# Kernel tuning notes

Hardware: AMD Instinct MI355X
Metric: run time of the kernel (lower is better)

## Reference

```python
import jax, jax.numpy as jnp
import numpy as np

USAGE_DECAY = 0.99
EPS = 1e-12


def _addressing(key, beta, gate, shift, gamma, prev_w, memory, half_shift):
    # key [B,M], beta/gate/gamma [B,1], shift [B,K], prev_w [B,N], memory [B,N,M]
    kn = key / (jnp.linalg.norm(key, axis=-1, keepdims=True) + EPS)
    mn = memory / (jnp.linalg.norm(memory, axis=-1, keepdims=True) + EPS)
    cos = jnp.einsum('bnm,bm->bn', mn, kn)                      # [B,N]
    beta_p = jax.nn.softplus(beta[:, 0])
    wc = jax.nn.softmax(beta_p[:, None] * cos, axis=-1)
    g = jax.nn.sigmoid(gate[:, 0])[:, None]
    wg = g * wc + (1.0 - g) * prev_w
    s = jax.nn.softmax(shift, axis=-1)                          # [B,K]
    K = shift.shape[-1]
    shifted = sum(s[:, k:k + 1] * jnp.roll(wg, k - half_shift, axis=-1) for k in range(K))
    gamma_p = 1.0 + jax.nn.softplus(gamma[:, 0])
    wt = (shifted + EPS) ** gamma_p[:, None]
    return wt / (wt.sum(axis=-1, keepdims=True) + EPS)


def _allocate(usage):
    # faithful to source: cumprod over zero-prepended shifted usage
    sorted_u = jnp.sort(usage, axis=-1)
    free = jnp.argsort(usage, axis=-1)
    shifted = jnp.concatenate([jnp.zeros_like(sorted_u[:, :1]), sorted_u[:, :-1]], axis=-1)
    aw = (1.0 - sorted_u) * jnp.cumprod(shifted, axis=-1)
    B = usage.shape[0]
    return jnp.zeros_like(usage).at[jnp.arange(B)[:, None], free].set(aw)


def _forward(ctrl, read_W, read_b, write_W, write_b,
             memory0, link0, precedence0, usage0, read_w0, write_w0):
    T, B, D = ctrl.shape
    N, M = memory0.shape[1], memory0.shape[2]
    RH, WH = read_w0.shape[1], write_w0.shape[1]
    rpl = read_W.shape[0] // RH   # M + K + 6
    wpl = write_W.shape[0] // WH  # 3M + K + 4
    K = rpl - M - 6
    half = K // 2
    eye = jnp.eye(N, dtype=memory0.dtype)

    def step(carry, ctrl_t):
        memory, link, prec, usage, read_w, write_w = carry
        rp = (ctrl_t @ read_W.T + read_b).reshape(B, RH, rpl)
        wp = (ctrl_t @ write_W.T + write_b).reshape(B, WH, wpl)

        # ---- write heads: content addr + allocation, erase/add, temporal links ----
        new_write = []
        for h in range(WH):
            p = wp[:, h]
            key = p[:, :M]
            beta = p[:, M:M + 1]
            gate = p[:, M + 1:M + 2]
            shift = p[:, M + 2:M + 2 + K]
            gamma = p[:, M + 2 + K:M + 3 + K]
            erase = jax.nn.sigmoid(p[:, M + 3 + K:2 * M + 3 + K])
            add = p[:, 2 * M + 3 + K:3 * M + 3 + K]
            a_gate = jax.nn.sigmoid(p[:, 3 * M + 3 + K:])          # [B,1]
            w_addr = _addressing(key, beta, gate, shift, gamma, write_w[:, h], memory, half)
            alloc = _allocate(usage)
            w = a_gate * alloc + (1.0 - a_gate) * w_addr           # [B,N]
            memory = memory * (1.0 - w[:, :, None] * erase[:, None, :]) + w[:, :, None] * add[:, None, :]
            link = (1.0 - w[:, :, None]) * link + prec[:, :, None] * w[:, None, :]
            link = link * (1.0 - eye)[None]
            # faithful to source: sum over dim 0 (batch)
            prec = (1.0 - w.sum(axis=0, keepdims=True)) * prec + w
            usage = jnp.clip(USAGE_DECAY * usage + w, 0.0, 1.0)
            new_write.append(w)
        write_w = jnp.stack(new_write, axis=1)

        # ---- read heads: content + forward/backward temporal link modes ----
        new_read, reads = [], []
        for h in range(RH):
            p = rp[:, h]
            key = p[:, :M]
            beta = p[:, M:M + 1]
            gate = p[:, M + 1:M + 2]
            shift = p[:, M + 2:M + 2 + K]
            gamma = p[:, M + 2 + K:M + 3 + K]
            pi = jax.nn.softmax(p[:, M + 3 + K:M + 6 + K], axis=-1)  # [B,3] back/content/fwd
            wc = _addressing(key, beta, gate, shift, gamma, read_w[:, h], memory, half)
            fwd = jnp.einsum('bn,bnk->bk', read_w[:, h], link)
            bwd = jnp.einsum('bn,bkn->bk', read_w[:, h], link)
            w = pi[:, 0:1] * bwd + pi[:, 1:2] * wc + pi[:, 2:3] * fwd
            new_read.append(w)
            reads.append(jnp.einsum('bn,bnm->bm', w, memory))
        read_w = jnp.stack(new_read, axis=1)
        reads = jnp.stack(reads, axis=1)                            # [B,RH,M]
        return (memory, link, prec, usage, read_w, write_w), reads

    carry0 = (memory0, link0, precedence0, usage0, read_w0, write_w0)
    _, reads = jax.lax.scan(step, carry0, ctrl)
    return reads  # [T,B,RH,M]


def setup_inputs() -> dict:
    key = jax.random.key(0)
    ks = jax.random.split(key, 8)
    T, B, D = 32, 4, 256
    N, M = 1024, 256
    RH, WH, K = 1, 1, 3
    rpl = M + K + 6
    wpl = 3 * M + K + 4
    ctrl = jax.random.normal(ks[0], (T, B, D), dtype=jnp.float32)
    read_W = jax.random.normal(ks[1], (RH * rpl, D), dtype=jnp.float32) * 0.05
    read_b = jnp.zeros((RH * rpl,), dtype=jnp.float32)
    write_W = jax.random.normal(ks[2], (WH * wpl, D), dtype=jnp.float32) * 0.05
    write_b = jnp.zeros((WH * wpl,), dtype=jnp.float32)
    memory0 = jax.random.normal(ks[3], (B, N, M), dtype=jnp.float32) * 0.1
    link0 = jnp.zeros((B, N, N), dtype=jnp.float32)
    precedence0 = jnp.zeros((B, N), dtype=jnp.float32)
    usage0 = jax.random.uniform(ks[4], (B, N), dtype=jnp.float32)
    read_w0 = jnp.zeros((B, RH, N), dtype=jnp.float32).at[:, :, 0].set(1.0)
    write_w0 = jnp.zeros((B, WH, N), dtype=jnp.float32).at[:, :, 0].set(1.0)
    return {"ctrl": ctrl, "read_W": read_W, "read_b": read_b,
            "write_W": write_W, "write_b": write_b, "memory0": memory0,
            "link0": link0, "precedence0": precedence0, "usage0": usage0,
            "read_w0": read_w0, "write_w0": write_w0}


def reference(ctrl, read_W, read_b, write_W, write_b, memory0, link0,
              precedence0, usage0, read_w0, write_w0):
    return _forward(ctrl, read_W, read_b, write_W, write_b,
                    memory0, link0, precedence0, usage0, read_w0, write_w0)
```

## Files before the change

### kernel.cpp

```cpp
#include <hip/hip_runtime.h>

#define GRID 128
#define TPB 256
#define SLICE 32
#define BB 4
#define DD 256
#define NN 1024
#define MM 256
#define KSH 3
#define RPL 265
#define WPL 775
#define TS 32
#define EPSF 1e-12f

struct KArgs {
    const float *ctrl, *rW, *rb, *wW, *wb;
    const float *memory0, *prec0, *read_w0, *write_w0;
    float *out;
    float *rp, *wp;
    float *cosr, *cosw, *wbuf, *rdw;
    float *csp, *dsp;
    float *rdp;
    unsigned *flagsA, *flagsB;
};

__device__ __forceinline__ float cload(const float* p){
    return __hip_atomic_load(p, __ATOMIC_RELAXED, __HIP_MEMORY_SCOPE_SYSTEM);
}
__device__ __forceinline__ void cstore(float* p, float v){
    __hip_atomic_store(p, v, __ATOMIC_RELAXED, __HIP_MEMORY_SCOPE_SYSTEM);
}

__device__ __forceinline__ float softplusf(float x){
    return fmaxf(x, 0.0f) + log1pf(expf(-fabsf(x)));
}
__device__ __forceinline__ float sigmoidf(float x){
    return 1.0f / (1.0f + expf(-x));
}

template <bool FENCE>
__device__ __forceinline__ void garrive(unsigned* flags, unsigned gen, int g, int tid){
    __syncthreads();
    if (tid == 0){
        if (FENCE) __builtin_amdgcn_fence(__ATOMIC_RELEASE, "agent");
        __hip_atomic_store(&flags[g*16], gen, __ATOMIC_RELAXED, __HIP_MEMORY_SCOPE_SYSTEM);
    }
}
template <bool FENCE>
__device__ __forceinline__ void gwait(unsigned* flags, unsigned gen, int tid){
    if (tid < 64){
        while (1){
            unsigned f0 = __hip_atomic_load(&flags[tid*16], __ATOMIC_RELAXED, __HIP_MEMORY_SCOPE_SYSTEM);
            unsigned f1 = __hip_atomic_load(&flags[(tid+64)*16], __ATOMIC_RELAXED, __HIP_MEMORY_SCOPE_SYSTEM);
            if (__all(f0 >= gen && f1 >= gen)) break;
            __builtin_amdgcn_s_sleep(1);
        }
    }
    __syncthreads();
    if (FENCE) __builtin_amdgcn_fence(__ATOMIC_ACQUIRE, "agent");
    asm volatile("" ::: "memory");
}

__device__ __forceinline__ float blk_sum(float v, float* s4, int tid){
    #pragma unroll
    for (int off = 32; off; off >>= 1) v += __shfl_down(v, off);
    if ((tid & 63) == 0) s4[tid >> 6] = v;
    __syncthreads();
    float r = s4[0] + s4[1] + s4[2] + s4[3];
    __syncthreads();
    return r;
}
__device__ __forceinline__ float blk_max(float v, float* s4, int tid){
    #pragma unroll
    for (int off = 32; off; off >>= 1) v = fmaxf(v, __shfl_down(v, off));
    if ((tid & 63) == 0) s4[tid >> 6] = v;
    __syncthreads();
    float r = fmaxf(fmaxf(s4[0], s4[1]), fmaxf(s4[2], s4[3]));
    __syncthreads();
    return r;
}
__device__ __forceinline__ float half_sum(float v, float* slots, int htid){
    #pragma unroll
    for (int off = 32; off; off >>= 1) v += __shfl_down(v, off);
    if ((htid & 63) == 0) slots[htid >> 6] = v;
    __syncthreads();
    float r = slots[0] + slots[1];
    __syncthreads();
    return r;
}

__device__ __forceinline__ void addr_core2(const float cosx[4], const float prev[4],
                                           const float* __restrict__ p,
                                           float* s4, float* wg, int tid,
                                           float out_wc[4]){
    float beta_p  = softplusf(p[MM]);
    float g       = sigmoidf(p[MM+1]);
    float s0r = p[MM+2], s1r = p[MM+3], s2r = p[MM+4];
    float smx = fmaxf(s0r, fmaxf(s1r, s2r));
    float e0 = expf(s0r-smx), e1 = expf(s1r-smx), e2 = expf(s2r-smx);
    float sden = e0+e1+e2;
    float s0 = e0/sden, s1 = e1/sden, s2 = e2/sden;
    float gamma_p = 1.0f + softplusf(p[MM+2+KSH]);
    float ev[4]; float ls = 0.0f;
    #pragma unroll
    for (int q = 0; q < 4; q++){ ev[q] = expf(beta_p*cosx[q] - beta_p); ls += ev[q]; }
    float bs = blk_sum(ls, s4, tid);
    float invb = 1.0f / bs;
    #pragma unroll
    for (int q = 0; q < 4; q++){
        int i = tid + q*256;
        wg[i] = g*(ev[q]*invb) + (1.0f-g)*prev[q];
    }
    __syncthreads();
    float wt[4]; float lps = 0.0f;
    #pragma unroll
    for (int q = 0; q < 4; q++){
        int i = tid + q*256;
        float sh = s0*wg[(i+1)&(NN-1)] + s1*wg[i] + s2*wg[(i-1)&(NN-1)];
        wt[q] = exp2f(gamma_p * log2f(sh + EPSF));
        lps += wt[q];
    }
    float ts = blk_sum(lps, s4, tid);
    float inv = 1.0f / (ts + EPSF);
    #pragma unroll
    for (int q = 0; q < 4; q++) out_wc[q] = wt[q] * inv;
    __syncthreads();
}

__device__ __forceinline__ void addr_half(const float cosx[8], const float prev[8],
                                          const float* __restrict__ p,
                                          float* swg, float* slots,
                                          int htid, float out_wc[8]){
    float beta_p  = softplusf(p[MM]);
    float g       = sigmoidf(p[MM+1]);
    float s0r = p[MM+2], s1r = p[MM+3], s2r = p[MM+4];
    float smx = fmaxf(s0r, fmaxf(s1r, s2r));
    float e0 = expf(s0r-smx), e1 = expf(s1r-smx), e2 = expf(s2r-smx);
    float sden = e0+e1+e2;
    float s0 = e0/sden, s1 = e1/sden, s2 = e2/sden;
    float gamma_p = 1.0f + softplusf(p[MM+2+KSH]);

    float ev[8]; float ls = 0.0f;
    #pragma unroll
    for (int q = 0; q < 8; q++){ ev[q] = expf(beta_p*cosx[q] - beta_p); ls += ev[q]; }
    float bs = half_sum(ls, slots, htid);
    float invb = 1.0f / bs;
    #pragma unroll
    for (int q = 0; q < 8; q++){
        int i = htid + q*128;
        swg[i] = g*(ev[q]*invb) + (1.0f-g)*prev[q];
    }
    __syncthreads();
    float wt[8]; float lps = 0.0f;
    #pragma unroll
    for (int q = 0; q < 8; q++){
        int i = htid + q*128;
        float sh = s0*swg[(i+1)&(NN-1)] + s1*swg[i] + s2*swg[(i-1)&(NN-1)];
        wt[q] = exp2f(gamma_p * log2f(sh + EPSF));
        lps += wt[q];
    }
    float ts2 = half_sum(lps, slots, htid);
    float inv = 1.0f / (ts2 + EPSF);
    #pragma unroll
    for (int q = 0; q < 8; q++) out_wc[q] = wt[q] * inv;
    __syncthreads();
}

__device__ __forceinline__ void tail_cos(const KArgs& a, int tnext, int b, int g, int ns0,
        float (*lmem)[MM], float (*skey)[MM],
        const float* lwn, const float* rdvec, int tid){
    if (rdvec){
        float accv = 0.f;
        #pragma unroll 8
        for (int j = 0; j < SLICE; j++) accv += rdvec[j]*lmem[j][tid];
        cstore(&a.rdp[(size_t)((tnext-1)&1)*GRID*MM + g*MM + tid], accv);
    }
    const float* kr = a.rp + (size_t)tnext*BB*RPL + (size_t)b*RPL;
    const bool hw = (tnext+1 <= TS-1);
    const float* kwp = a.wp + (size_t)(hw ? tnext+1 : tnext)*BB*WPL + (size_t)b*WPL;
    skey[0][tid] = kr[tid];
    skey[1][tid] = kwp[tid];
    __syncthreads();
    {
        const float* pw = a.wp + (size_t)tnext*BB*WPL + (size_t)b*WPL;
        float e = pw[MM+3+KSH + tid];
        float d = pw[2*MM+3+KSH + tid];
        #pragma unroll 8
        for (int j = 0; j < SLICE; j++){
            float w = lwn[j];
            lmem[j][tid] = lmem[j][tid]*(1.0f - w*e) + w*d;
        }
    }
    __syncthreads();
    {
        int j = tid >> 3, c = tid & 7;
        float dr=0.f, dw=0.f, nm=0.f, nr=0.f, nk=0.f;
        #pragma unroll
        for (int m = 0; m < 8; m++){
            int col = c*4 + m*32;
            float4 mv = *(const float4*)&lmem[j][col];
            float4 rv = *(const float4*)&skey[0][col];
            float4 wv = *(const float4*)&skey[1][col];
            dr += mv.x*rv.x + mv.y*rv.y + mv.z*rv.z + mv.w*rv.w;
            dw += mv.x*wv.x + mv.y*wv.y + mv.z*wv.z + mv.w*wv.w;
            nm += mv.x*mv.x + mv.y*mv.y + mv.z*mv.z + mv.w*mv.w;
            nr += rv.x*rv.x + rv.y*rv.y + rv.z*rv.z + rv.w*rv.w;
            nk += wv.x*wv.x + wv.y*wv.y + wv.z*wv.z + wv.w*wv.w;
        }
        #pragma unroll
        for (int off = 4; off; off >>= 1){
            dr += __shfl_down(dr, off); dw += __shfl_down(dw, off);
            nm += __shfl_down(nm, off); nr += __shfl_down(nr, off);
            nk += __shfl_down(nk, off);
        }
        if (c == 0){
            float sn = sqrtf(nm) + EPSF;
            int n = ns0 + j;
            cstore(&a.cosr[(size_t)(tnext&1)*BB*NN + b*NN + n], dr/(sn*(sqrtf(nr)+EPSF)));
            if (hw) cstore(&a.cosw[(size_t)((tnext+1)&1)*BB*NN + b*NN + n], dw/(sn*(sqrtf(nk)+EPSF)));
        }
    }
}

__device__ __forceinline__ void tail_links(const KArgs& a, int tnext, int g,
        float (*lA)[SLICE], float (*lW)[SLICE],
        const float* lwn, const float* rvec, const float* lprec, int tid){
    for (int p2 = tid; p2 < tnext*SLICE; p2 += TPB){
        int s = p2 >> 5, jj = p2 & 31;
        lA[s][jj] *= (1.0f - lwn[jj]);
    }
    __syncthreads();
    if (tid < SLICE){ lA[tnext][tid] = lprec[tid]; lW[tnext][tid] = lwn[tid]; }
    __syncthreads();
    int s = tid >> 3, c = tid & 7;
    if (s <= tnext){
        float pc = 0.f, pd = 0.f;
        #pragma unroll
        for (int q = 0; q < 4; q++){
            int jj = c*4 + q;
            float r = rvec[jj];
            pc += r*lA[s][jj];
            pd += r*lW[s][jj];
        }
        #pragma unroll
        for (int off = 4; off; off >>= 1){ pc += __shfl_down(pc, off); pd += __shfl_down(pd, off); }
        if (c == 0){
            cstore(&a.csp[(size_t)(tnext&1)*GRID*TS + g*TS + s], pc);
            cstore(&a.dsp[(size_t)(tnext&1)*GRID*TS + g*TS + s], pd);
        }
    }
}

__global__ void __launch_bounds__(TPB) kfull(KArgs a){
    const int g   = blockIdx.x;
    const int tid = threadIdx.x;
    const int wvi = tid >> 6, lane = tid & 63;
    const int b   = g >> 5;
    const int sl  = g & 31;
    const int ns0 = sl * SLICE;
    const int sq    = sl >> 3;
    const int sbase = (sl & 7) * 32;
    const int hbase = ns0 & 127;
    const int qsl   = ns0 >> 7;

    __shared__ __align__(16) float lmem[SLICE][MM];
    __shared__ __align__(16) float skey[2][MM];
    __shared__ __align__(16) float lA[TS][SLICE];
    __shared__ __align__(16) float lW[TS][SLICE];
    __shared__ float wgA[NN], wgB[NN];
    __shared__ float s8[8];
    __shared__ float scs[TS], sds[TS];
    __shared__ float lprec[SLICE], lr_old[SLICE], lw_old[SLICE];
    __shared__ float lrn[SLICE], lwn[SLICE], lbw[SLICE], lfw[SLICE];

    {
        const int tt = g >> 2;
        for (int o = tid; o < BB*DD; o += TPB) wgA[o] = a.ctrl[(size_t)tt*BB*DD + o];
        __syncthreads();
        for (int half = 0; half < 2; half++){
            int jc = (g & 3) + half*4;
            int j = jc*130 + tid;
            if (tid < 130 && j < RPL + WPL){
                const float* wrow; float bias; int isw, jj;
                if (j < RPL){ jj = j;       wrow = a.rW + (size_t)jj*DD; bias = a.rb[jj]; isw = 0; }
                else        { jj = j - RPL; wrow = a.wW + (size_t)jj*DD; bias = a.wb[jj]; isw = 1; }
                const float4* w4 = (const float4*)wrow;
                float a0 = bias, a1 = bias, a2 = bias, a3 = bias;
                for (int d = 0; d < DD/4; d++){
                    float4 wv = w4[d];
                    float4 c0 = *(const float4*)&wgA[0*DD + d*4];
                    float4 c1 = *(const float4*)&wgA[1*DD + d*4];
                    float4 c2 = *(const float4*)&wgA[2*DD + d*4];
                    float4 c3 = *(const float4*)&wgA[3*DD + d*4];
                    a0 += wv.x*c0.x + wv.y*c0.y + wv.z*c0.z + wv.w*c0.w;
                    a1 += wv.x*c1.x + wv.y*c1.y + wv.z*c1.z + wv.w*c1.w;
                    a2 += wv.x*c2.x + wv.y*c2.y + wv.z*c2.z + wv.w*c2.w;
                    a3 += wv.x*c3.x + wv.y*c3.y + wv.z*c3.z + wv.w*c3.w;
                }
                if (isw && jj >= MM+3+KSH && jj < 2*MM+3+KSH){
                    a0 = sigmoidf(a0); a1 = sigmoidf(a1); a2 = sigmoidf(a2); a3 = sigmoidf(a3);
                }
                if (!isw){
                    float* dst = a.rp + (size_t)tt*BB*RPL;
                    dst[0*RPL+jj]=a0; dst[1*RPL+jj]=a1; dst[2*RPL+jj]=a2; dst[3*RPL+jj]=a3;
                } else {
                    float* dst = a.wp + (size_t)tt*BB*WPL;
                    dst[0*WPL+jj]=a0; dst[1*WPL+jj]=a1; dst[2*WPL+jj]=a2; dst[3*WPL+jj]=a3;
                }
            }
        }
    }
    garrive<true>(a.flagsA, 1, g, tid);
    gwait<true>(a.flagsA, 1, tid);

    {
        const float* kw = a.wp + (size_t)b*WPL;
        const int m0 = lane*4;
        float k0=kw[m0], k1=kw[m0+1], k2=kw[m0+2], k3=kw[m0+3];
        float nk = k0*k0 + k1*k1 + k2*k2 + k3*k3;
        #pragma unroll
        for (int off = 32; off; off >>= 1) nk += __shfl_down(nk, off);
        nk = __shfl(nk, 0);
        float snk = sqrtf(nk) + EPSF;
        for (int rr = 0; rr < 8; rr++){
            int j = wvi*8 + rr, n = ns0 + j;
            float4 m4 = ((const float4*)a.memory0)[((size_t)(b*NN+n))*64 + lane];
            *(float4*)&lmem[j][m0] = m4;
            float dw = m4.x*k0 + m4.y*k1 + m4.z*k2 + m4.w*k3;
            float nm = m4.x*m4.x + m4.y*m4.y + m4.z*m4.z + m4.w*m4.w;
            #pragma unroll
            for (int off = 32; off; off >>= 1){ dw += __shfl_down(dw, off); nm += __shfl_down(nm, off); }
            if (lane == 0) cstore(&a.cosw[0*BB*NN + b*NN + n], dw / ((sqrtf(nm)+EPSF)*snk));
        }
        if (tid < SLICE){
            lprec[tid]  = a.prec0[b*NN + ns0 + tid];
            lr_old[tid] = a.read_w0[b*NN + ns0 + tid];
        }
    }
    garrive<false>(a.flagsA, 2, g, tid);
    gwait<false>(a.flagsA, 2, tid);

    {
        const float* p = a.wp + (size_t)b*WPL;
        float cosx[4], prev[4], wcf[4];
        #pragma unroll
        for (int q = 0; q < 4; q++){
            int i = tid + q*256;
            cosx[q] = cload(&a.cosw[0*BB*NN + b*NN + i]);
            prev[q] = a.write_w0[b*NN + i];
        }
        addr_core2(cosx, prev, p, s8, wgA, tid, wcf);
        float ag = sigmoidf(p[3*MM+3+KSH]);
        if (tid >= sbase && tid < sbase+32){
            int j = tid - sbase;
            float v = (1.0f - ag)*wcf[sq];
            lwn[j] = v;
            cstore(&a.wbuf[0*BB*NN + b*NN + ns0 + j], v);
        }
        __syncthreads();
        tail_cos(a, 0, b, g, ns0, lmem, skey, lwn, nullptr, tid);
        garrive<false>(a.flagsA, 3, g, tid);
        tail_links(a, 0, g, lA, lW, lwn, lr_old, lprec, tid);
        garrive<false>(a.flagsB, 1, g, tid);
        __syncthreads();
        if (tid < SLICE) lw_old[tid] = lwn[tid];
    }

    for (int t = 0; t < TS; t++){
        const int cur = t & 1, nxt = cur ^ 1;
        const int half = wvi >> 1, htid = tid & 127;
        gwait<false>(a.flagsA, 3 + t, tid);

        float cosx[8], prev[8];
        const float* addr_p;
        if (half == 0){
            addr_p = a.rp + (size_t)t*BB*RPL + (size_t)b*RPL;
            #pragma unroll
            for (int q = 0; q < 8; q++){
                int i = htid + q*128;
                cosx[q] = cload(&a.cosr[(size_t)cur*BB*NN + b*NN + i]);
                prev[q] = (t == 0) ? a.read_w0[b*NN + i]
                                   : cload(&a.rdw[(size_t)nxt*BB*NN + b*NN + i]);
            }
        } else {
            int tw = (t < TS-1) ? t+1 : t;
            addr_p = a.wp + (size_t)tw*BB*WPL + (size_t)b*WPL;
            #pragma unroll
            for (int q = 0; q < 8; q++){
                int i = htid + q*128;
                cosx[q] = cload(&a.cosw[(size_t)nxt*BB*NN + b*NN + i]);
                prev[q] = cload(&a.wbuf[(size_t)cur*BB*NN + b*NN + i]);
            }
        }
        if (tid < SLICE){
            float wsum = 0.f;
            #pragma unroll
            for (int bq = 0; bq < BB; bq++)
                wsum += cload(&a.wbuf[(size_t)cur*BB*NN + bq*NN + ns0 + tid]);
            lprec[tid] = (1.0f - wsum)*lprec[tid] + lw_old[tid];
        }

        float wcf[8];
        addr_half(cosx, prev, addr_p,
                  (half == 0) ? wgA : wgB,
                  (half == 0) ? &s8[0] : &s8[2],
                  htid, wcf);

        gwait<false>(a.flagsB, 1 + t, tid);

        {
            int s = tid >> 3, c = tid & 7;
            float pc = 0.f, pd = 0.f;
            if (s <= t){
                #pragma unroll
                for (int q = 0; q < 4; q++){
                    int slc = c + q*8;
                    pc += cload(&a.csp[(size_t)cur*GRID*TS + (b*32+slc)*TS + s]);
                    pd += cload(&a.dsp[(size_t)cur*GRID*TS + (b*32+slc)*TS + s]);
                }
            }
            float rdpv = 0.f;
            if (t > 0)
                rdpv = cload(&a.rdp[(size_t)nxt*GRID*MM + (b*32+(tid&31))*MM + sl*8 + (tid>>5)]);
            #pragma unroll
            for (int off = 4; off; off >>= 1){ pc += __shfl_down(pc, off); pd += __shfl_down(pd, off); }
            if (c == 0 && s <= t){ scs[s] = pc; sds[s] = pd; }
            if (t > 0){
                #pragma unroll
                for (int off = 16; off; off >>= 1) rdpv += __shfl_down(rdpv, off);
                if ((tid & 31) == 0) a.out[(size_t)(t-1)*BB*MM + b*MM + sl*8 + (tid>>5)] = rdpv;
            }
        }
        __syncthreads();
        if (tid < SLICE){
            float bwv = 0.f, fwv = 0.f, qq = 0.f;
            for (int s2 = 0; s2 <= t; s2++){
                float av = lA[s2][tid], wv = lW[s2][tid];
                qq  += av*wv;
                bwv += sds[s2]*av;
                fwv += scs[s2]*wv;
            }
            float corr = lr_old[tid]*qq;
            lbw[tid] = bwv - corr;
            lfw[tid] = fwv - corr;
        }
        __syncthreads();
        if (half == 0){
            float x0 = addr_p[MM+3+KSH], x1 = addr_p[MM+4+KSH], x2 = addr_p[MM+5+KSH];
            float mx = fmaxf(x0, fmaxf(x1, x2));
            float q0 = expf(x0-mx), q1 = expf(x1-mx), q2 = expf(x2-mx);
            float qs = q0+q1+q2;
            float pi0 = q0/qs, pi1 = q1/qs, pi2 = q2/qs;
            if (htid >= hbase && htid < hbase + 32){
                int j = htid - hbase;
                float v = pi0*lbw[j] + pi1*wcf[qsl] + pi2*lfw[j];
                lrn[j] = v;
                cstore(&a.rdw[(size_t)cur*BB*NN + b*NN + ns0 + j], v);
            }
        } else if (t < TS-1){
            float ag = sigmoidf(addr_p[3*MM+3+KSH]);
            if (htid >= hbase && htid < hbase + 32){
                int j = htid - hbase;
                float v = (1.0f - ag)*wcf[qsl];
                lwn[j] = v;
                cstore(&a.wbuf[(size_t)nxt*BB*NN + b*NN + ns0 + j], v);
            }
        }
        __syncthreads();

        if (t < TS-1){
            tail_cos(a, t+1, b, g, ns0, lmem, skey, lwn, lrn, tid);
            garrive<false>(a.flagsA, 4 + t, g, tid);
            tail_links(a, t+1, g, lA, lW, lwn, lrn, lprec, tid);
            garrive<false>(a.flagsB, 2 + t, g, tid);
            __syncthreads();
            if (tid < SLICE){ lr_old[tid] = lrn[tid]; lw_old[tid] = lwn[tid]; }
        } else {
            float accv = 0.f;
            #pragma unroll 8
            for (int j = 0; j < SLICE; j++) accv += lrn[j]*lmem[j][tid];
            cstore(&a.rdp[(size_t)1*GRID*MM + g*MM + tid], accv);
            garrive<false>(a.flagsB, 2 + t, g, tid);
        }
    }

    gwait<false>(a.flagsB, TS + 1, tid);
    {
        float v = cload(&a.rdp[(size_t)1*GRID*MM + (b*32+(tid&31))*MM + sl*8 + (tid>>5)]);
        #pragma unroll
        for (int off = 16; off; off >>= 1) v += __shfl_down(v, off);
        if ((tid & 31) == 0) a.out[(size_t)(TS-1)*BB*MM + b*MM + sl*8 + (tid>>5)] = v;
    }
}

extern "C" void kernel_launch(void* const* d_in, const int* in_sizes, int n_in,
                              void* d_out, int out_size, void* d_ws, size_t ws_size,
                              hipStream_t stream) {
    KArgs ka;
    ka.ctrl     = (const float*)d_in[0];
    ka.rW       = (const float*)d_in[1];
    ka.rb       = (const float*)d_in[2];
    ka.wW       = (const float*)d_in[3];
    ka.wb       = (const float*)d_in[4];
    ka.memory0  = (const float*)d_in[5];
    ka.prec0    = (const float*)d_in[7];
    ka.read_w0  = (const float*)d_in[9];
    ka.write_w0 = (const float*)d_in[10];
    ka.out      = (float*)d_out;

    float* ws = (float*)d_ws;
    size_t off = 0;
    auto alloc = [&](size_t n){ float* p = ws + off; off += n; return p; };
    ka.rp    = alloc((size_t)TS*BB*RPL);
    ka.wp    = alloc((size_t)TS*BB*WPL);
    ka.cosr  = alloc(2*(size_t)BB*NN);
    ka.cosw  = alloc(2*(size_t)BB*NN);
    ka.wbuf  = alloc(2*(size_t)BB*NN);
    ka.rdw   = alloc(2*(size_t)BB*NN);
    ka.csp   = alloc(2*(size_t)GRID*TS);
    ka.dsp   = alloc(2*(size_t)GRID*TS);
    ka.rdp   = alloc(2*(size_t)GRID*MM);
    unsigned* ubase = (unsigned*)(ws + off);
    ka.flagsA = ubase;
    ka.flagsB = ubase + GRID*16;
    size_t bar_bytes = (2*GRID*16) * sizeof(unsigned);

    hipMemsetAsync((void*)ubase, 0, bar_bytes, stream);
    void* params[] = { &ka };
    hipLaunchCooperativeKernel((const void*)kfull, dim3(GRID), dim3(TPB), params, 0, stream);
}
```

Measured before the change: 332.7 us.

## Cut block barriers and restructure per-step tail loops in persistent DNC kernel

Removes several __syncthreads by giving the addressing reductions separate shared slots and merging the link decay/insert passes into one loop. The read-vector partial product is fused into the memory erase/add update, which now uses float4 rows split across waves; this writes four partial rdp rows per block, and consumers sum them. The cosine computation is remapped to 32-lane reductions over rows, and the link readout is spread across all threads with a shuffle reduction instead of 32 threads looping. Link arrays are padded to 33 columns to avoid LDS bank conflicts. The cost is more global partial stores and loads, and relying on barriers being correctly placed after their removal.

```diff
diff --git a/kernel.cpp b/kernel.cpp
--- a/kernel.cpp
+++ b/kernel.cpp
@@ -12,6 +12,7 @@
 #define WPL 775
 #define TS 32
 #define EPSF 1e-12f
+#define SLP 33
 
 struct KArgs {
     const float *ctrl, *rW, *rb, *wW, *wb;
@@ -70,23 +71,13 @@
     __syncthreads();
     return r;
 }
-__device__ __forceinline__ float blk_max(float v, float* s4, int tid){
-    #pragma unroll
-    for (int off = 32; off; off >>= 1) v = fmaxf(v, __shfl_down(v, off));
-    if ((tid & 63) == 0) s4[tid >> 6] = v;
-    __syncthreads();
-    float r = fmaxf(fmaxf(s4[0], s4[1]), fmaxf(s4[2], s4[3]));
-    __syncthreads();
-    return r;
-}
-__device__ __forceinline__ float half_sum(float v, float* slots, int htid){
+
+__device__ __forceinline__ float half_sum1(float v, float* slot2, int htid){
     #pragma unroll
     for (int off = 32; off; off >>= 1) v += __shfl_down(v, off);
-    if ((htid & 63) == 0) slots[htid >> 6] = v;
-    __syncthreads();
-    float r = slots[0] + slots[1];
-    __syncthreads();
-    return r;
+    if ((htid & 63) == 0) slot2[htid >> 6] = v;
+    __syncthreads();
+    return slot2[0] + slot2[1];
 }
 
 __device__ __forceinline__ void addr_core2(const float cosx[4], const float prev[4],
@@ -129,7 +120,7 @@
 
 __device__ __forceinline__ void addr_half(const float cosx[8], const float prev[8],
                                           const float* __restrict__ p,
-                                          float* swg, float* slots,
+                                          float* swg, float* slot_bs, float* slot_ts,
                                           int htid, float out_wc[8]){
     float beta_p  = softplusf(p[MM]);
     float g       = sigmoidf(p[MM+1]);
@@ -143,7 +134,7 @@
     float ev[8]; float ls = 0.0f;
     #pragma unroll
     for (int q = 0; q < 8; q++){ ev[q] = expf(beta_p*cosx[q] - beta_p); ls += ev[q]; }
-    float bs = half_sum(ls, slots, htid);
+    float bs = half_sum1(ls, slot_bs, htid);
     float invb = 1.0f / bs;
     #pragma unroll
     for (int q = 0; q < 8; q++){
@@ -159,23 +150,17 @@
         wt[q] = exp2f(gamma_p * log2f(sh + EPSF));
         lps += wt[q];
     }
-    float ts2 = half_sum(lps, slots, htid);
+    float ts2 = half_sum1(lps, slot_ts, htid);
     float inv = 1.0f / (ts2 + EPSF);
     #pragma unroll
     for (int q = 0; q < 8; q++) out_wc[q] = wt[q] * inv;
-    __syncthreads();
-}
-
-__device__ __forceinline__ void tail_cos(const KArgs& a, int tnext, int b, int g, int ns0,
+}
+
+__device__ __forceinline__ void tail_cos2(const KArgs& a, int tnext, int b, int g, int ns0,
         float (*lmem)[MM], float (*skey)[MM],
-        const float* lwn, const float* rdvec, int tid){
-    if (rdvec){
-        float accv = 0.f;
-        #pragma unroll 8
-        for (int j = 0; j < SLICE; j++) accv += rdvec[j]*lmem[j][tid];
-        cstore(&a.rdp[(size_t)((tnext-1)&1)*GRID*MM + g*MM + tid], accv);
-    }
-    const float* kr = a.rp + (size_t)tnext*BB*RPL + (size_t)b*RPL;
+        const float* lwn, const float* rdvec,
+        int tid, int wvi){
+    const float* kr  = a.rp + (size_t)tnext*BB*RPL + (size_t)b*RPL;
     const bool hw = (tnext+1 <= TS-1);
     const float* kwp = a.wp + (size_t)(hw ? tnext+1 : tnext)*BB*WPL + (size_t)b*WPL;
     skey[0][tid] = kr[tid];
@@ -183,54 +168,81 @@
     __syncthreads();
     {
         const float* pw = a.wp + (size_t)tnext*BB*WPL + (size_t)b*WPL;
-        float e = pw[MM+3+KSH + tid];
-        float d = pw[2*MM+3+KSH + tid];
-        #pragma unroll 8
-        for (int j = 0; j < SLICE; j++){
+        const int quad = tid & 63;
+        float eX[4], dX[4];
+        #pragma unroll
+        for (int k = 0; k < 4; k++){
+            eX[k] = pw[MM+3+KSH   + quad*4 + k];
+            dX[k] = pw[2*MM+3+KSH + quad*4 + k];
+        }
+        float4 acc = make_float4(0.f,0.f,0.f,0.f);
+        #pragma unroll
+        for (int it = 0; it < 8; it++){
+            int j = wvi + it*4;
             float w = lwn[j];
-            lmem[j][tid] = lmem[j][tid]*(1.0f - w*e) + w*d;
+            float4 mv = *(float4*)&lmem[j][quad*4];
+            if (rdvec){
+                float r = rdvec[j];
+                acc.x += r*mv.x; acc.y += r*mv.y; acc.z += r*mv.z; acc.w += r*mv.w;
+            }
+            mv.x = mv.x*(1.0f - w*eX[0]) + w*dX[0];
+            mv.y = mv.y*(1.0f - w*eX[1]) + w*dX[1];
+            mv.z = mv.z*(1.0f - w*eX[2]) + w*dX[2];
+            mv.w = mv.w*(1.0f - w*eX[3]) + w*dX[3];
+            *(float4*)&lmem[j][quad*4] = mv;
+        }
+        if (rdvec){
+            float* base = a.rdp + (size_t)((tnext-1)&1)*GRID*4*MM + (size_t)g*4*MM + wvi*MM + quad*4;
+            cstore(base+0, acc.x); cstore(base+1, acc.y);
+            cstore(base+2, acc.z); cstore(base+3, acc.w);
         }
     }
     __syncthreads();
     {
-        int j = tid >> 3, c = tid & 7;
-        float dr=0.f, dw=0.f, nm=0.f, nr=0.f, nk=0.f;
+        const int cc = tid & 31, jb = tid >> 5;
+        float nr = 0.f, nk = 0.f;
         #pragma unroll
         for (int m = 0; m < 8; m++){
-            int col = c*4 + m*32;
-            float4 mv = *(const float4*)&lmem[j][col];
-            float4 rv = *(const float4*)&skey[0][col];
-            float4 wv = *(const float4*)&skey[1][col];
-            dr += mv.x*rv.x + mv.y*rv.y + mv.z*rv.z + mv.w*rv.w;
-            dw += mv.x*wv.x + mv.y*wv.y + mv.z*wv.z + mv.w*wv.w;
-            nm += mv.x*mv.x + mv.y*mv.y + mv.z*mv.z + mv.w*mv.w;
-            nr += rv.x*rv.x + rv.y*rv.y + rv.z*rv.z + rv.w*rv.w;
-            nk += wv.x*wv.x + wv.y*wv.y + wv.z*wv.z + wv.w*wv.w;
-        }
-        #pragma unroll
-        for (int off = 4; off; off >>= 1){
-            dr += __shfl_down(dr, off); dw += __shfl_down(dw, off);
-            nm += __shfl_down(nm, off); nr += __shfl_down(nr, off);
-            nk += __shfl_down(nk, off);
-        }
-        if (c == 0){
-            float sn = sqrtf(nm) + EPSF;
-            int n = ns0 + j;
-            cstore(&a.cosr[(size_t)(tnext&1)*BB*NN + b*NN + n], dr/(sn*(sqrtf(nr)+EPSF)));
-            if (hw) cstore(&a.cosw[(size_t)((tnext+1)&1)*BB*NN + b*NN + n], dw/(sn*(sqrtf(nk)+EPSF)));
-        }
-    }
-}
-
-__device__ __forceinline__ void tail_links(const KArgs& a, int tnext, int g,
-        float (*lA)[SLICE], float (*lW)[SLICE],
+            int col = cc + m*32;
+            float rv = skey[0][col], wv = skey[1][col];
+            nr += rv*rv; nk += wv*wv;
+        }
+        #pragma unroll
+        for (int off = 16; off; off >>= 1){ nr += __shfl_down(nr, off); nk += __shfl_down(nk, off); }
+        #pragma unroll
+        for (int rb = 0; rb < 4; rb++){
+            int j = jb + rb*8;
+            float dr = 0.f, dw = 0.f, nm = 0.f;
+            #pragma unroll
+            for (int m = 0; m < 8; m++){
+                int col = cc + m*32;
+                float mv = lmem[j][col];
+                dr += mv*skey[0][col];
+                dw += mv*skey[1][col];
+                nm += mv*mv;
+            }
+            #pragma unroll
+            for (int off = 16; off; off >>= 1){
+                dr += __shfl_down(dr, off); dw += __shfl_down(dw, off); nm += __shfl_down(nm, off);
+            }
+            if (cc == 0){
+                float sn = sqrtf(nm) + EPSF;
+                int n = ns0 + j;
+                cstore(&a.cosr[(size_t)(tnext&1)*BB*NN + b*NN + n], dr/(sn*(sqrtf(nr)+EPSF)));
+                if (hw) cstore(&a.cosw[(size_t)((tnext+1)&1)*BB*NN + b*NN + n], dw/(sn*(sqrtf(nk)+EPSF)));
+            }
+        }
+    }
+}
+
+__device__ __forceinline__ void tail_links2(const KArgs& a, int tnext, int g,
+        float (*lA)[SLP], float (*lW)[SLP],
         const float* lwn, const float* rvec, const float* lprec, int tid){
-    for (int p2 = tid; p2 < tnext*SLICE; p2 += TPB){
+    for (int p2 = tid; p2 < (tnext+1)*SLICE; p2 += TPB){
         int s = p2 >> 5, jj = p2 & 31;
-        lA[s][jj] *= (1.0f - lwn[jj]);
-    }
-    __syncthreads();
-    if (tid < SLICE){ lA[tnext][tid] = lprec[tid]; lW[tnext][tid] = lwn[tid]; }
+        if (s == tnext){ lA[s][jj] = lprec[jj]; lW[s][jj] = lwn[jj]; }
+        else            lA[s][jj] *= (1.0f - lwn[jj]);
+    }
     __syncthreads();
     int s = tid >> 3, c = tid & 7;
     if (s <= tnext){
@@ -265,8 +277,8 @@
 
     __shared__ __align__(16) float lmem[SLICE][MM];
     __shared__ __align__(16) float skey[2][MM];
-    __shared__ __align__(16) float lA[TS][SLICE];
-    __shared__ __align__(16) float lW[TS][SLICE];
+    __shared__ float lA[TS][SLP];
+    __shared__ float lW[TS][SLP];
     __shared__ float wgA[NN], wgB[NN];
     __shared__ float s8[8];
     __shared__ float scs[TS], sds[TS];
@@ -357,13 +369,11 @@
             lwn[j] = v;
             cstore(&a.wbuf[0*BB*NN + b*NN + ns0 + j], v);
         }
-        __syncthreads();
-        tail_cos(a, 0, b, g, ns0, lmem, skey, lwn, nullptr, tid);
+        tail_cos2(a, 0, b, g, ns0, lmem, skey, lwn, nullptr, tid, wvi);
+        if (tid < SLICE) lw_old[tid] = lwn[tid];
         garrive<false>(a.flagsA, 3, g, tid);
-        tail_links(a, 0, g, lA, lW, lwn, lr_old, lprec, tid);
+        tail_links2(a, 0, g, lA, lW, lwn, lr_old, lprec, tid);
         garrive<false>(a.flagsB, 1, g, tid);
-        __syncthreads();
-        if (tid < SLICE) lw_old[tid] = lwn[tid];
     }
 
     for (int t = 0; t < TS; t++){
@@ -404,6 +414,7 @@
         addr_half(cosx, prev, addr_p,
                   (half == 0) ? wgA : wgB,
                   (half == 0) ? &s8[0] : &s8[2],
+                  (half == 0) ? &s8[4] : &s8[6],
                   htid, wcf);
 
         gwait<false>(a.flagsB, 1 + t, tid);
@@ -420,8 +431,12 @@
                 }
             }
             float rdpv = 0.f;
-            if (t > 0)
-                rdpv = cload(&a.rdp[(size_t)nxt*GRID*MM + (b*32+(tid&31))*MM + sl*8 + (tid>>5)]);
+            if (t > 0){
+                int slc = tid & 31, ci = tid >> 5;
+                const float* base = a.rdp + (size_t)nxt*GRID*4*MM + (size_t)(b*32+slc)*4*MM + sl*8 + ci;
+                #pragma unroll
+                for (int f = 0; f < 4; f++) rdpv += cload(base + f*MM);
+            }
             #pragma unroll
             for (int off = 4; off; off >>= 1){ pc += __shfl_down(pc, off); pd += __shfl_down(pd, off); }
             if (c == 0 && s <= t){ scs[s] = pc; sds[s] = pd; }
@@ -432,17 +447,22 @@
             }
         }
         __syncthreads();
-        if (tid < SLICE){
+        {
+            int j2 = tid >> 3, c2 = tid & 7;
             float bwv = 0.f, fwv = 0.f, qq = 0.f;
-            for (int s2 = 0; s2 <= t; s2++){
-                float av = lA[s2][tid], wv = lW[s2][tid];
-                qq  += av*wv;
-                bwv += sds[s2]*av;
-                fwv += scs[s2]*wv;
-            }
-            float corr = lr_old[tid]*qq;
-            lbw[tid] = bwv - corr;
-            lfw[tid] = fwv - corr;
+            for (int s2 = c2; s2 <= t; s2 += 8){
+                float av = lA[s2][j2], wv = lW[s2][j2];
+                qq += av*wv; bwv += sds[s2]*av; fwv += scs[s2]*wv;
+            }
+            #pragma unroll
+            for (int off = 4; off; off >>= 1){
+                bwv += __shfl_down(bwv, off); fwv += __shfl_down(fwv, off); qq += __shfl_down(qq, off);
+            }
+            if (c2 == 0){
+                float corr = lr_old[j2]*qq;
+                lbw[j2] = bwv - corr;
+                lfw[j2] = fwv - corr;
+            }
         }
         __syncthreads();
         if (half == 0){
@@ -466,30 +486,41 @@
                 cstore(&a.wbuf[(size_t)nxt*BB*NN + b*NN + ns0 + j], v);
             }
         }
-        __syncthreads();
 
         if (t < TS-1){
-            tail_cos(a, t+1, b, g, ns0, lmem, skey, lwn, lrn, tid);
+            tail_cos2(a, t+1, b, g, ns0, lmem, skey, lwn, lrn, tid, wvi);
+            if (tid < SLICE){ lr_old[tid] = lrn[tid]; lw_old[tid] = lwn[tid]; }
             garrive<false>(a.flagsA, 4 + t, g, tid);
-            tail_links(a, t+1, g, lA, lW, lwn, lrn, lprec, tid);
+            tail_links2(a, t+1, g, lA, lW, lwn, lrn, lprec, tid);
             garrive<false>(a.flagsB, 2 + t, g, tid);
+        } else {
             __syncthreads();
-            if (tid < SLICE){ lr_old[tid] = lrn[tid]; lw_old[tid] = lwn[tid]; }
-        } else {
-            float accv = 0.f;
-            #pragma unroll 8
-            for (int j = 0; j < SLICE; j++) accv += lrn[j]*lmem[j][tid];
-            cstore(&a.rdp[(size_t)1*GRID*MM + g*MM + tid], accv);
+            const int quad = tid & 63;
+            float4 acc = make_float4(0.f,0.f,0.f,0.f);
+            #pragma unroll
+            for (int it = 0; it < 8; it++){
+                int j = wvi + it*4;
+                float r = lrn[j];
+                float4 mv = *(float4*)&lmem[j][quad*4];
+                acc.x += r*mv.x; acc.y += r*mv.y; acc.z += r*mv.z; acc.w += r*mv.w;
+            }
+            float* base = a.rdp + (size_t)1*GRID*4*MM + (size_t)g*4*MM + wvi*MM + quad*4;
+            cstore(base+0, acc.x); cstore(base+1, acc.y);
+            cstore(base+2, acc.z); cstore(base+3, acc.w);
             garrive<false>(a.flagsB, 2 + t, g, tid);
         }
     }
 
     gwait<false>(a.flagsB, TS + 1, tid);
     {
-        float v = cload(&a.rdp[(size_t)1*GRID*MM + (b*32+(tid&31))*MM + sl*8 + (tid>>5)]);
+        int slc = tid & 31, ci = tid >> 5;
+        const float* base = a.rdp + (size_t)1*GRID*4*MM + (size_t)(b*32+slc)*4*MM + sl*8 + ci;
+        float v = 0.f;
+        #pragma unroll
+        for (int f = 0; f < 4; f++) v += cload(base + f*MM);
         #pragma unroll
         for (int off = 16; off; off >>= 1) v += __shfl_down(v, off);
-        if ((tid & 31) == 0) a.out[(size_t)(TS-1)*BB*MM + b*MM + sl*8 + (tid>>5)] = v;
+        if ((tid & 31) == 0) a.out[(size_t)(TS-1)*BB*MM + b*MM + sl*8 + ci] = v;
     }
 }
 
@@ -519,7 +550,7 @@
     ka.rdw   = alloc(2*(size_t)BB*NN);
     ka.csp   = alloc(2*(size_t)GRID*TS);
     ka.dsp   = alloc(2*(size_t)GRID*TS);
-    ka.rdp   = alloc(2*(size_t)GRID*MM);
+    ka.rdp   = alloc(2*(size_t)GRID*4*MM);
     unsigned* ubase = (unsigned*)(ws + off);
     ka.flagsA = ubase;
     ka.flagsB = ubase + GRID*16;
```

Result: slower. 383.6 us (+15.3%).

## Halve grid to 64 blocks of 512 threads with 64-row memory slices

Applied to the files above, without the earlier changes.

Repartitions the persistent cooperative kernel from 128 blocks of 256 threads to 64 blocks of 512 threads, each owning a 64-row memory slice. Read and write addressing now run on two 256-thread teams in parallel. Grid barriers poll half as many flags, and the cross-block partial reductions shrink. The flagsB wait and the global loads of link and read partials are moved before addressing, and the read-vector accumulation is fused into the memory update loop. The cost is more shared memory per block and fewer CUs in use.

```diff
diff --git a/kernel.cpp b/kernel.cpp
--- a/kernel.cpp
+++ b/kernel.cpp
@@ -1,8 +1,8 @@
 #include <hip/hip_runtime.h>
 
-#define GRID 128
-#define TPB 256
-#define SLICE 32
+#define GRID 64
+#define TPB 512
+#define SLICE 64
 #define BB 4
 #define DD 256
 #define NN 1024
@@ -51,8 +51,7 @@
     if (tid < 64){
         while (1){
             unsigned f0 = __hip_atomic_load(&flags[tid*16], __ATOMIC_RELAXED, __HIP_MEMORY_SCOPE_SYSTEM);
-            unsigned f1 = __hip_atomic_load(&flags[(tid+64)*16], __ATOMIC_RELAXED, __HIP_MEMORY_SCOPE_SYSTEM);
-            if (__all(f0 >= gen && f1 >= gen)) break;
+            if (__all(f0 >= gen)) break;
             __builtin_amdgcn_s_sleep(1);
         }
     }
@@ -61,38 +60,18 @@
     asm volatile("" ::: "memory");
 }
 
-__device__ __forceinline__ float blk_sum(float v, float* s4, int tid){
+__device__ __forceinline__ float team_sum(float v, float* slot4, int ttid){
     #pragma unroll
     for (int off = 32; off; off >>= 1) v += __shfl_down(v, off);
-    if ((tid & 63) == 0) s4[tid >> 6] = v;
-    __syncthreads();
-    float r = s4[0] + s4[1] + s4[2] + s4[3];
-    __syncthreads();
-    return r;
-}
-__device__ __forceinline__ float blk_max(float v, float* s4, int tid){
-    #pragma unroll
-    for (int off = 32; off; off >>= 1) v = fmaxf(v, __shfl_down(v, off));
-    if ((tid & 63) == 0) s4[tid >> 6] = v;
-    __syncthreads();
-    float r = fmaxf(fmaxf(s4[0], s4[1]), fmaxf(s4[2], s4[3]));
-    __syncthreads();
-    return r;
-}
-__device__ __forceinline__ float half_sum(float v, float* slots, int htid){
-    #pragma unroll
-    for (int off = 32; off; off >>= 1) v += __shfl_down(v, off);
-    if ((htid & 63) == 0) slots[htid >> 6] = v;
-    __syncthreads();
-    float r = slots[0] + slots[1];
-    __syncthreads();
-    return r;
-}
-
-__device__ __forceinline__ void addr_core2(const float cosx[4], const float prev[4],
-                                           const float* __restrict__ p,
-                                           float* s4, float* wg, int tid,
-                                           float out_wc[4]){
+    if ((ttid & 63) == 0) slot4[ttid >> 6] = v;
+    __syncthreads();
+    return slot4[0] + slot4[1] + slot4[2] + slot4[3];
+}
+
+__device__ __forceinline__ void addr_team(const float cosx[4], const float prev[4],
+                                          const float* __restrict__ p,
+                                          float* swg, float* slot_bs, float* slot_ts,
+                                          int ttid, float out_wc[4]){
     float beta_p  = softplusf(p[MM]);
     float g       = sigmoidf(p[MM+1]);
     float s0r = p[MM+2], s1r = p[MM+3], s2r = p[MM+4];
@@ -104,94 +83,56 @@
     float ev[4]; float ls = 0.0f;
     #pragma unroll
     for (int q = 0; q < 4; q++){ ev[q] = expf(beta_p*cosx[q] - beta_p); ls += ev[q]; }
-    float bs = blk_sum(ls, s4, tid);
+    float bs = team_sum(ls, slot_bs, ttid);
     float invb = 1.0f / bs;
     #pragma unroll
     for (int q = 0; q < 4; q++){
-        int i = tid + q*256;
-        wg[i] = g*(ev[q]*invb) + (1.0f-g)*prev[q];
+        int i = ttid + q*256;
+        swg[i] = g*(ev[q]*invb) + (1.0f-g)*prev[q];
     }
     __syncthreads();
     float wt[4]; float lps = 0.0f;
     #pragma unroll
     for (int q = 0; q < 4; q++){
-        int i = tid + q*256;
-        float sh = s0*wg[(i+1)&(NN-1)] + s1*wg[i] + s2*wg[(i-1)&(NN-1)];
-        wt[q] = exp2f(gamma_p * log2f(sh + EPSF));
-        lps += wt[q];
-    }
-    float ts = blk_sum(lps, s4, tid);
-    float inv = 1.0f / (ts + EPSF);
-    #pragma unroll
-    for (int q = 0; q < 4; q++) out_wc[q] = wt[q] * inv;
-    __syncthreads();
-}
-
-__device__ __forceinline__ void addr_half(const float cosx[8], const float prev[8],
-                                          const float* __restrict__ p,
-                                          float* swg, float* slots,
-                                          int htid, float out_wc[8]){
-    float beta_p  = softplusf(p[MM]);
-    float g       = sigmoidf(p[MM+1]);
-    float s0r = p[MM+2], s1r = p[MM+3], s2r = p[MM+4];
-    float smx = fmaxf(s0r, fmaxf(s1r, s2r));
-    float e0 = expf(s0r-smx), e1 = expf(s1r-smx), e2 = expf(s2r-smx);
-    float sden = e0+e1+e2;
-    float s0 = e0/sden, s1 = e1/sden, s2 = e2/sden;
-    float gamma_p = 1.0f + softplusf(p[MM+2+KSH]);
-
-    float ev[8]; float ls = 0.0f;
-    #pragma unroll
-    for (int q = 0; q < 8; q++){ ev[q] = expf(beta_p*cosx[q] - beta_p); ls += ev[q]; }
-    float bs = half_sum(ls, slots, htid);
-    float invb = 1.0f / bs;
-    #pragma unroll
-    for (int q = 0; q < 8; q++){
-        int i = htid + q*128;
-        swg[i] = g*(ev[q]*invb) + (1.0f-g)*prev[q];
-    }
-    __syncthreads();
-    float wt[8]; float lps = 0.0f;
-    #pragma unroll
-    for (int q = 0; q < 8; q++){
-        int i = htid + q*128;
+        int i = ttid + q*256;
         float sh = s0*swg[(i+1)&(NN-1)] + s1*swg[i] + s2*swg[(i-1)&(NN-1)];
         wt[q] = exp2f(gamma_p * log2f(sh + EPSF));
         lps += wt[q];
     }
-    float ts2 = half_sum(lps, slots, htid);
+    float ts2 = team_sum(lps, slot_ts, ttid);
     float inv = 1.0f / (ts2 + EPSF);
     #pragma unroll
-    for (int q = 0; q < 8; q++) out_wc[q] = wt[q] * inv;
-    __syncthreads();
+    for (int q = 0; q < 4; q++) out_wc[q] = wt[q] * inv;
 }
 
 __device__ __forceinline__ void tail_cos(const KArgs& a, int tnext, int b, int g, int ns0,
-        float (*lmem)[MM], float (*skey)[MM],
+        float (*lmem)[MM], float (*skey)[MM], float* wred,
         const float* lwn, const float* rdvec, int tid){
-    if (rdvec){
-        float accv = 0.f;
-        #pragma unroll 8
-        for (int j = 0; j < SLICE; j++) accv += rdvec[j]*lmem[j][tid];
-        cstore(&a.rdp[(size_t)((tnext-1)&1)*GRID*MM + g*MM + tid], accv);
-    }
     const float* kr = a.rp + (size_t)tnext*BB*RPL + (size_t)b*RPL;
     const bool hw = (tnext+1 <= TS-1);
     const float* kwp = a.wp + (size_t)(hw ? tnext+1 : tnext)*BB*WPL + (size_t)b*WPL;
-    skey[0][tid] = kr[tid];
-    skey[1][tid] = kwp[tid];
+    if (tid < 256) skey[0][tid] = kr[tid];
+    else           skey[1][tid-256] = kwp[tid-256];
     __syncthreads();
     {
+        const int col = tid & 255, rg = tid >> 8;
         const float* pw = a.wp + (size_t)tnext*BB*WPL + (size_t)b*WPL;
-        float e = pw[MM+3+KSH + tid];
-        float d = pw[2*MM+3+KSH + tid];
+        float e = pw[MM+3+KSH + col];
+        float d = pw[2*MM+3+KSH + col];
+        float accv = 0.f;
         #pragma unroll 8
-        for (int j = 0; j < SLICE; j++){
+        for (int k = 0; k < 32; k++){
+            int j = rg*32 + k;
             float w = lwn[j];
-            lmem[j][tid] = lmem[j][tid]*(1.0f - w*e) + w*d;
-        }
-    }
-    __syncthreads();
+            float mv = lmem[j][col];
+            if (rdvec) accv += rdvec[j]*mv;
+            lmem[j][col] = mv*(1.0f - w*e) + w*d;
+        }
+        if (rdvec) wred[rg*256 + col] = accv;
+    }
+    __syncthreads();
+    if (rdvec && tid < 256)
+        cstore(&a.rdp[(size_t)((tnext-1)&1)*GRID*MM + g*MM + tid], wred[tid] + wred[256+tid]);
     {
         int j = tid >> 3, c = tid & 7;
         float dr=0.f, dw=0.f, nm=0.f, nr=0.f, nk=0.f;
@@ -226,7 +167,7 @@
         float (*lA)[SLICE], float (*lW)[SLICE],
         const float* lwn, const float* rvec, const float* lprec, int tid){
     for (int p2 = tid; p2 < tnext*SLICE; p2 += TPB){
-        int s = p2 >> 5, jj = p2 & 31;
+        int s = p2 >> 6, jj = p2 & 63;
         lA[s][jj] *= (1.0f - lwn[jj]);
     }
     __syncthreads();
@@ -236,8 +177,8 @@
     if (s <= tnext){
         float pc = 0.f, pd = 0.f;
         #pragma unroll
-        for (int q = 0; q < 4; q++){
-            int jj = c*4 + q;
+        for (int q = 0; q < 8; q++){
+            int jj = c*8 + q;
             float r = rvec[jj];
             pc += r*lA[s][jj];
             pd += r*lW[s][jj];
@@ -255,32 +196,29 @@
     const int g   = blockIdx.x;
     const int tid = threadIdx.x;
     const int wvi = tid >> 6, lane = tid & 63;
-    const int b   = g >> 5;
-    const int sl  = g & 31;
+    const int b   = g >> 4;
+    const int sl  = g & 15;
     const int ns0 = sl * SLICE;
-    const int sq    = sl >> 3;
-    const int sbase = (sl & 7) * 32;
-    const int hbase = ns0 & 127;
-    const int qsl   = ns0 >> 7;
+    const int qsl   = ns0 >> 8;
+    const int hbase = ns0 & 255;
 
     __shared__ __align__(16) float lmem[SLICE][MM];
     __shared__ __align__(16) float skey[2][MM];
     __shared__ __align__(16) float lA[TS][SLICE];
     __shared__ __align__(16) float lW[TS][SLICE];
-    __shared__ float wgA[NN], wgB[NN];
-    __shared__ float s8[8];
+    __shared__ __align__(16) float wgA[NN], wgB[NN];
+    __shared__ float s16[16];
     __shared__ float scs[TS], sds[TS];
     __shared__ float lprec[SLICE], lr_old[SLICE], lw_old[SLICE];
     __shared__ float lrn[SLICE], lwn[SLICE], lbw[SLICE], lfw[SLICE];
 
     {
-        const int tt = g >> 2;
+        const int tt = g >> 1, hp = g & 1;
         for (int o = tid; o < BB*DD; o += TPB) wgA[o] = a.ctrl[(size_t)tt*BB*DD + o];
         __syncthreads();
-        for (int half = 0; half < 2; half++){
-            int jc = (g & 3) + half*4;
-            int j = jc*130 + tid;
-            if (tid < 130 && j < RPL + WPL){
+        for (int jo = tid; jo < 520; jo += TPB){
+            int j = hp*520 + jo;
+            if (j < RPL + WPL){
                 const float* wrow; float bias; int isw, jj;
                 if (j < RPL){ jj = j;       wrow = a.rW + (size_t)jj*DD; bias = a.rb[jj]; isw = 0; }
                 else        { jj = j - RPL; wrow = a.wW + (size_t)jj*DD; bias = a.wb[jj]; isw = 1; }
@@ -341,24 +279,26 @@
     gwait<false>(a.flagsA, 2, tid);
 
     {
+        const int half = wvi >> 2, ttid = tid & 255;
         const float* p = a.wp + (size_t)b*WPL;
         float cosx[4], prev[4], wcf[4];
         #pragma unroll
         for (int q = 0; q < 4; q++){
-            int i = tid + q*256;
+            int i = ttid + q*256;
             cosx[q] = cload(&a.cosw[0*BB*NN + b*NN + i]);
             prev[q] = a.write_w0[b*NN + i];
         }
-        addr_core2(cosx, prev, p, s8, wgA, tid, wcf);
+        addr_team(cosx, prev, p, (half==0)?wgA:wgB,
+                  (half==0)?&s16[0]:&s16[8], (half==0)?&s16[4]:&s16[12], ttid, wcf);
         float ag = sigmoidf(p[3*MM+3+KSH]);
-        if (tid >= sbase && tid < sbase+32){
-            int j = tid - sbase;
-            float v = (1.0f - ag)*wcf[sq];
+        if (half == 0 && ttid >= hbase && ttid < hbase + SLICE){
+            int j = ttid - hbase;
+            float v = (1.0f - ag)*wcf[qsl];
             lwn[j] = v;
             cstore(&a.wbuf[0*BB*NN + b*NN + ns0 + j], v);
         }
         __syncthreads();
-        tail_cos(a, 0, b, g, ns0, lmem, skey, lwn, nullptr, tid);
+        tail_cos(a, 0, b, g, ns0, lmem, skey, wgB, lwn, nullptr, tid);
         garrive<false>(a.flagsA, 3, g, tid);
         tail_links(a, 0, g, lA, lW, lwn, lr_old, lprec, tid);
         garrive<false>(a.flagsB, 1, g, tid);
@@ -368,16 +308,16 @@
 
     for (int t = 0; t < TS; t++){
         const int cur = t & 1, nxt = cur ^ 1;
-        const int half = wvi >> 1, htid = tid & 127;
+        const int half = wvi >> 2, ttid = tid & 255;
         gwait<false>(a.flagsA, 3 + t, tid);
 
-        float cosx[8], prev[8];
+        float cosx[4], prev[4];
         const float* addr_p;
         if (half == 0){
             addr_p = a.rp + (size_t)t*BB*RPL + (size_t)b*RPL;
             #pragma unroll
-            for (int q = 0; q < 8; q++){
-                int i = htid + q*128;
+            for (int q = 0; q < 4; q++){
+                int i = ttid + q*256;
                 cosx[q] = cload(&a.cosr[(size_t)cur*BB*NN + b*NN + i]);
                 prev[q] = (t == 0) ? a.read_w0[b*NN + i]
                                    : cload(&a.rdw[(size_t)nxt*BB*NN + b*NN + i]);
@@ -386,11 +326,31 @@
             int tw = (t < TS-1) ? t+1 : t;
             addr_p = a.wp + (size_t)tw*BB*WPL + (size_t)b*WPL;
             #pragma unroll
-            for (int q = 0; q < 8; q++){
-                int i = htid + q*128;
+            for (int q = 0; q < 4; q++){
+                int i = ttid + q*256;
                 cosx[q] = cload(&a.cosw[(size_t)nxt*BB*NN + b*NN + i]);
                 prev[q] = cload(&a.wbuf[(size_t)cur*BB*NN + b*NN + i]);
             }
+        }
+
+        gwait<false>(a.flagsB, 1 + t, tid);
+
+        float cv[2] = {0,0}, dv[2] = {0,0};
+        {
+            int s = tid >> 3, c = tid & 7;
+            if (s <= t){
+                #pragma unroll
+                for (int q = 0; q < 2; q++){
+                    int slc = c + q*8;
+                    cv[q] = cload(&a.csp[(size_t)cur*GRID*TS + (b*16+slc)*TS + s]);
+                    dv[q] = cload(&a.dsp[(size_t)cur*GRID*TS + (b*16+slc)*TS + s]);
+                }
+            }
+        }
+        float rdpv = 0.f;
+        if (t > 0 && tid < 256){
+            int grp = tid >> 4, slc = tid & 15;
+            rdpv = cload(&a.rdp[(size_t)nxt*GRID*MM + (size_t)(b*16+slc)*MM + sl*16 + grp]);
         }
         if (tid < SLICE){
             float wsum = 0.f;
@@ -400,35 +360,21 @@
             lprec[tid] = (1.0f - wsum)*lprec[tid] + lw_old[tid];
         }
 
-        float wcf[8];
-        addr_half(cosx, prev, addr_p,
-                  (half == 0) ? wgA : wgB,
-                  (half == 0) ? &s8[0] : &s8[2],
-                  htid, wcf);
-
-        gwait<false>(a.flagsB, 1 + t, tid);
+        float wcf[4];
+        addr_team(cosx, prev, addr_p, (half==0)?wgA:wgB,
+                  (half==0)?&s16[0]:&s16[8], (half==0)?&s16[4]:&s16[12], ttid, wcf);
 
         {
             int s = tid >> 3, c = tid & 7;
-            float pc = 0.f, pd = 0.f;
-            if (s <= t){
-                #pragma unroll
-                for (int q = 0; q < 4; q++){
-                    int slc = c + q*8;
-                    pc += cload(&a.csp[(size_t)cur*GRID*TS + (b*32+slc)*TS + s]);
-                    pd += cload(&a.dsp[(size_t)cur*GRID*TS + (b*32+slc)*TS + s]);
-                }
-            }
-            float rdpv = 0.f;
-            if (t > 0)
-                rdpv = cload(&a.rdp[(size_t)nxt*GRID*MM + (b*32+(tid&31))*MM + sl*8 + (tid>>5)]);
+            float pc = cv[0]+cv[1];
+            float pd = dv[0]+dv[1];
             #pragma unroll
             for (int off = 4; off; off >>= 1){ pc += __shfl_down(pc, off); pd += __shfl_down(pd, off); }
             if (c == 0 && s <= t){ scs[s] = pc; sds[s] = pd; }
-            if (t > 0){
+            if (t > 0 && tid < 256){
                 #pragma unroll
-                for (int off = 16; off; off >>= 1) rdpv += __shfl_down(rdpv, off);
-                if ((tid & 31) == 0) a.out[(size_t)(t-1)*BB*MM + b*MM + sl*8 + (tid>>5)] = rdpv;
+                for (int off = 8; off; off >>= 1) rdpv += __shfl_down(rdpv, off);
+                if ((tid & 15) == 0) a.out[(size_t)(t-1)*BB*MM + b*MM + sl*16 + (tid>>4)] = rdpv;
             }
         }
         __syncthreads();
@@ -451,16 +397,16 @@
             float q0 = expf(x0-mx), q1 = expf(x1-mx), q2 = expf(x2-mx);
             float qs = q0+q1+q2;
             float pi0 = q0/qs, pi1 = q1/qs, pi2 = q2/qs;
-            if (htid >= hbase && htid < hbase + 32){
-                int j = htid - hbase;
+            if (ttid >= hbase && ttid < hbase + SLICE){
+                int j = ttid - hbase;
                 float v = pi0*lbw[j] + pi1*wcf[qsl] + pi2*lfw[j];
                 lrn[j] = v;
                 cstore(&a.rdw[(size_t)cur*BB*NN + b*NN + ns0 + j], v);
             }
         } else if (t < TS-1){
             float ag = sigmoidf(addr_p[3*MM+3+KSH]);
-            if (htid >= hbase && htid < hbase + 32){
-                int j = htid - hbase;
+            if (ttid >= hbase && ttid < hbase + SLICE){
+                int j = ttid - hbase;
                 float v = (1.0f - ag)*wcf[qsl];
                 lwn[j] = v;
                 cstore(&a.wbuf[(size_t)nxt*BB*NN + b*NN + ns0 + j], v);
@@ -469,27 +415,35 @@
         __syncthreads();
 
         if (t < TS-1){
-            tail_cos(a, t+1, b, g, ns0, lmem, skey, lwn, lrn, tid);
+            tail_cos(a, t+1, b, g, ns0, lmem, skey, wgB, lwn, lrn, tid);
             garrive<false>(a.flagsA, 4 + t, g, tid);
             tail_links(a, t+1, g, lA, lW, lwn, lrn, lprec, tid);
             garrive<false>(a.flagsB, 2 + t, g, tid);
             __syncthreads();
             if (tid < SLICE){ lr_old[tid] = lrn[tid]; lw_old[tid] = lwn[tid]; }
         } else {
+            const int col = tid & 255, rg = tid >> 8;
             float accv = 0.f;
             #pragma unroll 8
-            for (int j = 0; j < SLICE; j++) accv += lrn[j]*lmem[j][tid];
-            cstore(&a.rdp[(size_t)1*GRID*MM + g*MM + tid], accv);
+            for (int k = 0; k < 32; k++){
+                int j = rg*32 + k;
+                accv += lrn[j]*lmem[j][col];
+            }
+            wgB[rg*256 + col] = accv;
+            __syncthreads();
+            if (tid < 256)
+                cstore(&a.rdp[(size_t)1*GRID*MM + g*MM + tid], wgB[tid] + wgB[256+tid]);
             garrive<false>(a.flagsB, 2 + t, g, tid);
         }
     }
 
     gwait<false>(a.flagsB, TS + 1, tid);
-    {
-        float v = cload(&a.rdp[(size_t)1*GRID*MM + (b*32+(tid&31))*MM + sl*8 + (tid>>5)]);
-        #pragma unroll
-        for (int off = 16; off; off >>= 1) v += __shfl_down(v, off);
-        if ((tid & 31) == 0) a.out[(size_t)(TS-1)*BB*MM + b*MM + sl*8 + (tid>>5)] = v;
+    if (tid < 256){
+        int grp = tid >> 4, slc = tid & 15;
+        float v = cload(&a.rdp[(size_t)1*GRID*MM + (size_t)(b*16+slc)*MM + sl*16 + grp]);
+        #pragma unroll
+        for (int off = 8; off; off >>= 1) v += __shfl_down(v, off);
+        if ((tid & 15) == 0) a.out[(size_t)(TS-1)*BB*MM + b*MM + sl*16 + grp] = v;
     }
 }
 
```

New measurement: 380.0 us. 1.14x slower.
